# Kernel tuning notes

Hardware: AMD Instinct MI355X
Metric: run time of the kernel (lower is better)

## Reference

```python
import jax, jax.numpy as jnp
from jax import lax
import numpy as np

T, B, C, H, L, K = 512, 32, 512, 512, 2, 2  # time, batch, in_feat, hidden, layers, kernel


def setup_inputs() -> dict:
    key = jax.random.key(0)
    k0, k1, k2 = jax.random.split(key, 3)
    x = jax.random.normal(k0, (T, B, C), dtype=jnp.float32)
    # per layer: [n_dir=2, n_gate=4 (z,f,o,i), H, Cin, K] conv weights and [2,4,H] biases
    w0 = jax.random.normal(k1, (2, 4, H, C, K), dtype=jnp.float32) * 0.05
    b0 = jnp.zeros((2, 4, H), dtype=jnp.float32)
    w1 = jax.random.normal(k2, (2, 4, H, 2 * H, K), dtype=jnp.float32) * 0.05
    b1 = jnp.zeros((2, 4, H), dtype=jnp.float32)
    return {"x": x, "w0": w0, "b0": b0, "w1": w1, "b1": b1}


def _conv(x, w, b):
    # x: [B, Cin, T], w: [H, Cin, K]; left-pad K-1 zeros == torch cat([zeros, x]) + VALID conv
    y = lax.conv_general_dilated(x, w, (1,), [(K - 1, 0)],
                                 dimension_numbers=("NCH", "OIH", "NCH"))
    return y + b[None, :, None]


def _qrnn_layer(x, W, b, reverse):
    # x: [B, Cin, T]; W: [4, H, Cin, K]; b: [4, H]
    if reverse:
        x = x[:, :, ::-1]  # note: original code does NOT flip the output back
    z = jnp.tanh(_conv(x, W[0], b[0]))
    f = jax.nn.sigmoid(_conv(x, W[1], b[1]))  # eval-mode zoneout: 1-(1-sigmoid)=sigmoid
    o = jax.nn.sigmoid(_conv(x, W[2], b[2]))
    i = jax.nn.sigmoid(_conv(x, W[3], b[3]))
    iz = i * z
    f_t = jnp.moveaxis(f, 2, 0)   # [T, B, H]
    iz_t = jnp.moveaxis(iz, 2, 0)

    def step(c, fi):
        ft, izt = fi
        c = ft * c + izt  # IFO pooling recurrence
        return c, c

    _, cs = lax.scan(step, jnp.zeros(f_t.shape[1:], f.dtype), (f_t, iz_t))
    c = jnp.moveaxis(cs, 0, 2)  # [B, H, T]
    return o * c


def _forward(x, w0, b0, w1, b1):
    h = jnp.transpose(x, (1, 2, 0))  # [T,B,C] -> [B,C,T]
    h_lasts = []
    for W, bb in ((w0, b0), (w1, b1)):
        d0 = _qrnn_layer(h, W[0], bb[0], False)
        d1 = _qrnn_layer(h, W[1], bb[1], True)
        t_last = h.shape[2] - 2  # lengths.fill_(T-1); t_last = lengths - 1 = T-2 (faithful)
        h_lasts.append(jnp.concatenate([d0[:, :, t_last], d1[:, :, 0]], axis=1))  # [B, 2H]
        h = jnp.concatenate([d0, d1], axis=1)  # [B, 2H, T]
    output = jnp.transpose(h, (2, 0, 1))  # [T, B, 2H]
    h_n = jnp.stack(h_lasts, axis=0)      # [L, B, 2H]
    return output, h_n


def reference(x, w0, b0, w1, b1):
    return _forward(x, w0, b0, w1, b1)
```

## Files before the change

### kernel.cpp

```cpp
#include <hip/hip_runtime.h>
#include <cstddef>
#include <cstdint>

#define Tn 512
#define Bn 32
#define Hn 512
static const size_t PLANE = 8388608;

typedef float f32x4 __attribute__((ext_vector_type(4)));
typedef __bf16 bf16x8 __attribute__((ext_vector_type(8)));
typedef _Float16 h2 __attribute__((ext_vector_type(2)));

__device__ __forceinline__ float sigm(float x) { return 1.0f / (1.0f + __expf(-x)); }
__device__ __forceinline__ float tanh_fast(float x) { return 2.0f / (1.0f + __expf(-2.0f * x)) - 1.0f; }
__device__ __forceinline__ unsigned short f2bf(float f) {
    unsigned int u = __float_as_uint(f);
    u += 0x7FFF + ((u >> 16) & 1);
    return (unsigned short)(u >> 16);
}


__global__ __launch_bounds__(256) void conv_x(const float* __restrict__ x,
                                              unsigned short* __restrict__ xbf) {
    const int i = blockIdx.x * 256 + threadIdx.x;
    const int c8 = i & 63;
    const int tp = (i >> 6) % 514;
    const int b  = (i >> 6) / 514;
    unsigned short v[8];
    if (tp == 0 || tp == 513) {
#pragma unroll
        for (int j = 0; j < 8; ++j) v[j] = 0;
    } else {
        const float* s = x + ((size_t)(tp - 1) * Bn + b) * 512 + c8 * 8;
#pragma unroll
        for (int j = 0; j < 8; ++j) v[j] = f2bf(s[j]);
    }
    unsigned short* d = xbf + ((size_t)b * 514 + tp) * 512 + c8 * 8;
    *(uint4*)d = *(const uint4*)v;
}

__global__ __launch_bounds__(256) void conv_w(const float* __restrict__ src,
                                              unsigned short* __restrict__ dst,
                                              int Cin, int total) {
    const int i = blockIdx.x * 256 + threadIdx.x;
    if (i >= total) return;
    const int K = 2 * Cin;
    const int dm2 = i / K;
    const int kp = i - dm2 * K;
    const int dir = dm2 >> 11;
    const int mp = dm2 & 2047;
    const int o = mp >> 2;
    const int g = mp & 3;
    const int tap = (kp >= Cin) ? 1 : 0;
    const int c = kp - tap * Cin;
    dst[i] = f2bf(src[((((size_t)dir * 4 + g) * 512 + o) * Cin + c) * 2 + tap]);
}

__global__ __launch_bounds__(256) void zero_h1pad(unsigned short* __restrict__ h1bf) {
    const int i = blockIdx.x * 256 + threadIdx.x;
    const int c = i & 1023;
    const int b = (i >> 10) & 31;
    const int tp = (i >> 15) ? 513 : 0;
    h1bf[((size_t)b * 514 + tp) * 1024 + c] = 0;
}

template <int CIN>
__global__ __launch_bounds__(256) void gate_gemm_bf16(
    const unsigned short* __restrict__ Wbf,
    const unsigned short* __restrict__ Xbf,
    const float* __restrict__ bias,
    h2* __restrict__ fiz,
    _Float16* __restrict__ osb,
    int dir)
{
    __shared__ __align__(16) unsigned char smem[32768];
    unsigned short* As = (unsigned short*)smem;
    unsigned short* Bs = (unsigned short*)(smem + 16384);

    const int tid = threadIdx.x;
    const int lane = tid & 63;
    const int wave = tid >> 6;
    const int n0 = blockIdx.x * 128;
    const int m0 = blockIdx.y * 128;
    const int wm = (wave & 1) * 64;
    const int wn = (wave >> 1) * 64;

    const unsigned short* pA[4];
    const unsigned short* pB0[4];
    unsigned short* ldst[8];
#pragma unroll
    for (int r = 0; r < 4; ++r) {
        const int q = r * 256 + tid;
        const int row = q >> 3;
        const int j = q & 7;
        const int kk = j ^ ((row >> 1) & 7);
        pA[r] = Wbf + (size_t)(m0 + row) * (2 * CIN) + kk * 8;
        const int n = n0 + row;
        const int t = n & 511;
        const int b = n >> 9;
        const int tp0 = dir ? (513 - t) : t;
        pB0[r] = Xbf + ((size_t)b * 514 + tp0) * CIN + kk * 8;
        ldst[r] = As + (size_t)q * 8;
        ldst[r + 4] = Bs + (size_t)q * 8;
    }
    const int dstep = dir ? -CIN : CIN;

    int offA[2][4], offB[2][4];
#pragma unroll
    for (int kh = 0; kh < 2; ++kh) {
        const int jr = (lane >> 4) + kh * 4;
#pragma unroll
        for (int f = 0; f < 4; ++f) {
            const int ma = wm + f * 16 + (lane & 15);
            offA[kh][f] = ma * 64 + (jr ^ ((ma >> 1) & 7)) * 8;
            const int nb = wn + f * 16 + (lane & 15);
            offB[kh][f] = nb * 64 + (jr ^ ((nb >> 1) & 7)) * 8;
        }
    }

    f32x4 acc[4][4] = {};

    auto mfma_stage = [&]() {
#pragma unroll
        for (int kh = 0; kh < 2; ++kh) {
            bf16x8 af[4], bfr[4];
#pragma unroll
            for (int f = 0; f < 4; ++f) {
                af[f] = *(const bf16x8*)&As[offA[kh][f]];
                bfr[f] = *(const bf16x8*)&Bs[offB[kh][f]];
            }
#pragma unroll
            for (int fm = 0; fm < 4; ++fm)
#pragma unroll
                for (int fn = 0; fn < 4; ++fn)
                    acc[fm][fn] = __builtin_amdgcn_mfma_f32_16x16x32_bf16(
                        af[fm], bfr[fn], acc[fm][fn], 0, 0, 0);
        }
    };

#define GL(P, D) __builtin_amdgcn_global_load_lds( \
        (const __attribute__((address_space(1))) unsigned int*)(P), \
        (__attribute__((address_space(3))) unsigned int*)(D), 16, 0, 0)

#pragma unroll
    for (int tap = 0; tap < 2; ++tap) {
        const unsigned short* a0 = pA[0] + tap * CIN;
        const unsigned short* a1 = pA[1] + tap * CIN;
        const unsigned short* a2 = pA[2] + tap * CIN;
        const unsigned short* a3 = pA[3] + tap * CIN;
        const unsigned short* b0 = pB0[0] + tap * dstep;
        const unsigned short* b1 = pB0[1] + tap * dstep;
        const unsigned short* b2 = pB0[2] + tap * dstep;
        const unsigned short* b3 = pB0[3] + tap * dstep;
#pragma unroll
        for (int s = 0; s < CIN / 64; ++s) {
            GL(a0, ldst[0]); GL(a1, ldst[1]);
            GL(a2, ldst[2]); GL(a3, ldst[3]);
            GL(b0, ldst[4]); GL(b1, ldst[5]);
            GL(b2, ldst[6]); GL(b3, ldst[7]);
            __builtin_amdgcn_s_waitcnt(0);
            __syncthreads();
            mfma_stage();
            __syncthreads();
            a0 += 64; a1 += 64; a2 += 64; a3 += 64;
            b0 += 64; b1 += 64; b2 += 64; b3 += 64;
        }
    }
#undef GL

    const int q = lane >> 4;
    const int o0 = blockIdx.y * 32;
    float Bz[4], Bf[4], Bo[4], Bi[4];
#pragma unroll
    for (int fm = 0; fm < 4; ++fm) {
        const int o = o0 + (wm >> 2) + fm * 4 + q;
        Bz[fm] = bias[o];
        Bf[fm] = bias[512 + o];
        Bo[fm] = bias[1024 + o];
        Bi[fm] = bias[1536 + o];
    }
    h2* Lfiz = (h2*)smem;
    _Float16* Los = (_Float16*)(smem + 18432);
#pragma unroll
    for (int fm = 0; fm < 4; ++fm) {
        const int ol = (wm >> 2) + fm * 4 + q;
#pragma unroll
        for (int fn = 0; fn < 4; ++fn) {
            f32x4 v = acc[fm][fn];
            const float f  = sigm(v.y + Bf[fm]);
            const float iz = sigm(v.w + Bi[fm]) * tanh_fast(v.x + Bz[fm]);
            const float os = sigm(v.z + Bo[fm]);
            const int nl = wn + fn * 16 + (lane & 15);
            h2 p; p.x = (_Float16)f; p.y = (_Float16)iz;
            Lfiz[nl * 36 + ol] = p;
            Los[nl * 40 + ol] = (_Float16)os;
        }
    }
    __syncthreads();
#pragma unroll
    for (int l = 0; l < 4; ++l) {
        const int idx = l * 256 + tid;
        const int row = idx >> 3;
        const int col = idx & 7;
        uint4 v = *(const uint4*)((const unsigned char*)smem + row * 144 + col * 16);
        ((uint4*)(fiz + (size_t)(n0 + row) * 512 + o0))[col] = v;
    }
#pragma unroll
    for (int l = 0; l < 2; ++l) {
        const int idx = l * 256 + tid;
        const int row = idx >> 2;
        const int col = idx & 3;
        uint4 v = *(const uint4*)((const unsigned char*)smem + 18432 + row * 80 + col * 16);
        ((uint4*)(osb + (size_t)(n0 + row) * 512 + o0))[col] = v;
    }
}


__global__ __launch_bounds__(256) void scan_A(
    const h2* __restrict__ fiz,
    float* __restrict__ Fsum, float* __restrict__ Ssum)
{
    const int idx = blockIdx.x * 256 + threadIdx.x;
    const int o = idx & 511;
    const int b = (idx >> 9) & 31;
    const int chunk = idx >> 14;
    float F = 1.0f, S = 0.0f;
    const int tbase = chunk * 64;
    for (int tt = 0; tt < 64; ++tt) {
        const h2 v = fiz[((size_t)(b * 512 + tbase + tt)) * 512 + o];
        const float f = (float)v.x;
        const float iz = (float)v.y;
        F *= f;
        S = f * S + iz;
    }
    Fsum[idx] = F;
    Ssum[idx] = S;
}

__global__ __launch_bounds__(256) void scan_B(
    const float* __restrict__ Fsum, const float* __restrict__ Ssum,
    float* __restrict__ cstart)
{
    const int i = blockIdx.x * 256 + threadIdx.x;
    float c = 0.0f;
    for (int ch = 0; ch < 8; ++ch) {
        cstart[ch * 16384 + i] = c;
        c = Fsum[ch * 16384 + i] * c + Ssum[ch * 16384 + i];
    }
}

__global__ __launch_bounds__(256) void scan_C(
    const h2* __restrict__ fiz, const _Float16* __restrict__ osb,
    const float* __restrict__ cstart, float* __restrict__ out,
    unsigned short* __restrict__ h1bf,
    float* __restrict__ hn, int isLayer2, int dirH)
{
    const int idx = blockIdx.x * 256 + threadIdx.x;
    const int o = idx & 511;
    const int b = (idx >> 9) & 31;
    const int chunk = idx >> 14;
    float c = cstart[idx];
    const int tbase = chunk * 64;
    for (int tt = 0; tt < 64; ++tt) {
        const int t = tbase + tt;
        const size_t idxg = ((size_t)(b * 512 + t)) * 512 + o;
        const h2 v = fiz[idxg];
        const float f = (float)v.x;
        const float iz = (float)v.y;
        const float os = (float)osb[idxg];
        c = f * c + iz;
        const float outv = os * c;
        if (isLayer2) {
            out[((size_t)t * Bn + b) * 1024 + dirH + o] = outv;
        } else {
            h1bf[((size_t)b * 514 + (t + 1)) * 1024 + dirH + o] = f2bf(outv);
        }
        const bool isLast = (dirH == 0) ? (t == Tn - 2) : (t == 0);
        if (isLast) hn[(size_t)b * 1024 + dirH + o] = outv;
    }
}

extern "C" void kernel_launch(void* const* d_in, const int* in_sizes, int n_in,
                              void* d_out, int out_size, void* d_ws, size_t ws_size,
                              hipStream_t stream) {
    const float* x  = (const float*)d_in[0];
    const float* w0 = (const float*)d_in[1];
    const float* b0 = (const float*)d_in[2];
    const float* w1 = (const float*)d_in[3];
    const float* b1 = (const float*)d_in[4];
    float* out = (float*)d_out;
    float* ws = (float*)d_ws;

    h2* fiz        = (h2*)ws;
    _Float16* osb  = (_Float16*)(ws + PLANE);
    float* Fsum    = ws + PLANE + PLANE / 2;
    float* Ssum    = Fsum + 131072;
    float* cst     = Ssum + 131072;
    unsigned short* xbf  = (unsigned short*)(cst + 131072);
    unsigned short* h1bf = xbf + (size_t)32 * 514 * 512;
    unsigned short* w0bf = h1bf + (size_t)32 * 514 * 1024;
    unsigned short* w1bf = w0bf + (size_t)2 * 2048 * 1024;
    float* hn = out + 16777216;

    conv_x<<<4112, 256, 0, stream>>>(x, xbf);
    conv_w<<<16384, 256, 0, stream>>>(w0, w0bf, 512, 4194304);
    conv_w<<<32768, 256, 0, stream>>>(w1, w1bf, 1024, 8388608);
    zero_h1pad<<<256, 256, 0, stream>>>(h1bf);

    const dim3 gg(128, 16);

    gate_gemm_bf16<512><<<gg, 256, 0, stream>>>(w0bf, xbf, b0, fiz, osb, 0);
    scan_A<<<512, 256, 0, stream>>>(fiz, Fsum, Ssum);
    scan_B<<<64, 256, 0, stream>>>(Fsum, Ssum, cst);
    scan_C<<<512, 256, 0, stream>>>(fiz, osb, cst, out, h1bf, hn, 0, 0);
    gate_gemm_bf16<512><<<gg, 256, 0, stream>>>(w0bf + (size_t)2048 * 1024, xbf, b0 + 2048, fiz, osb, 1);
    scan_A<<<512, 256, 0, stream>>>(fiz, Fsum, Ssum);
    scan_B<<<64, 256, 0, stream>>>(Fsum, Ssum, cst);
    scan_C<<<512, 256, 0, stream>>>(fiz, osb, cst, out, h1bf, hn, 0, 512);
    gate_gemm_bf16<1024><<<gg, 256, 0, stream>>>(w1bf, h1bf, b1, fiz, osb, 0);
    scan_A<<<512, 256, 0, stream>>>(fiz, Fsum, Ssum);
    scan_B<<<64, 256, 0, stream>>>(Fsum, Ssum, cst);
    scan_C<<<512, 256, 0, stream>>>(fiz, osb, cst, out, h1bf, hn + 32768, 1, 0);
    gate_gemm_bf16<1024><<<gg, 256, 0, stream>>>(w1bf + (size_t)2048 * 2048, h1bf, b1 + 2048, fiz, osb, 1);
    scan_A<<<512, 256, 0, stream>>>(fiz, Fsum, Ssum);
    scan_B<<<64, 256, 0, stream>>>(Fsum, Ssum, cst);
    scan_C<<<512, 256, 0, stream>>>(fiz, osb, cst, out, h1bf, hn + 32768, 1, 512);
}
```

Baseline: 696.4 us.

## Batch both directions per layer and fuse chunk-scan reduction into gate GEMM

```diff
diff --git a/kernel.cpp b/kernel.cpp
--- a/kernel.cpp
+++ b/kernel.cpp
@@ -39,11 +39,16 @@
     *(uint4*)d = *(const uint4*)v;
 }
 
-__global__ __launch_bounds__(256) void conv_w(const float* __restrict__ src,
-                                              unsigned short* __restrict__ dst,
-                                              int Cin, int total) {
-    const int i = blockIdx.x * 256 + threadIdx.x;
-    if (i >= total) return;
+__global__ __launch_bounds__(256) void conv_w2(const float* __restrict__ w0,
+                                               const float* __restrict__ w1,
+                                               unsigned short* __restrict__ w0bf,
+                                               unsigned short* __restrict__ w1bf) {
+    int i = blockIdx.x * 256 + threadIdx.x;
+    const float* src;
+    unsigned short* dst;
+    int Cin;
+    if (i < 4194304) { src = w0; dst = w0bf; Cin = 512; }
+    else { i -= 4194304; src = w1; dst = w1bf; Cin = 1024; }
     const int K = 2 * Cin;
     const int dm2 = i / K;
     const int kp = i - dm2 * K;
@@ -71,7 +76,8 @@
     const float* __restrict__ bias,
     h2* __restrict__ fiz,
     _Float16* __restrict__ osb,
-    int dir)
+    float* __restrict__ Fsum,
+    float* __restrict__ Ssum)
 {
     __shared__ __align__(16) unsigned char smem[32768];
     unsigned short* As = (unsigned short*)smem;
@@ -81,9 +87,12 @@
     const int lane = tid & 63;
     const int wave = tid >> 6;
     const int n0 = blockIdx.x * 128;
-    const int m0 = blockIdx.y * 128;
+    const int dir = blockIdx.y >> 4;
+    const int m0 = (blockIdx.y & 15) * 128;
     const int wm = (wave & 1) * 64;
     const int wn = (wave >> 1) * 64;
+
+    const unsigned short* Wb = Wbf + (size_t)dir * 2048 * 2 * CIN;
 
     const unsigned short* pA[4];
     const unsigned short* pB0[4];
@@ -94,7 +103,7 @@
         const int row = q >> 3;
         const int j = q & 7;
         const int kk = j ^ ((row >> 1) & 7);
-        pA[r] = Wbf + (size_t)(m0 + row) * (2 * CIN) + kk * 8;
+        pA[r] = Wb + (size_t)(m0 + row) * (2 * CIN) + kk * 8;
         const int n = n0 + row;
         const int t = n & 511;
         const int b = n >> 9;
@@ -169,15 +178,16 @@
 #undef GL
 
     const int q = lane >> 4;
-    const int o0 = blockIdx.y * 32;
+    const int o0 = (blockIdx.y & 15) * 32;
+    const float* bb = bias + dir * 2048;
     float Bz[4], Bf[4], Bo[4], Bi[4];
 #pragma unroll
     for (int fm = 0; fm < 4; ++fm) {
         const int o = o0 + (wm >> 2) + fm * 4 + q;
-        Bz[fm] = bias[o];
-        Bf[fm] = bias[512 + o];
-        Bo[fm] = bias[1024 + o];
-        Bi[fm] = bias[1536 + o];
+        Bz[fm] = bb[o];
+        Bf[fm] = bb[512 + o];
+        Bo[fm] = bb[1024 + o];
+        Bi[fm] = bb[1536 + o];
     }
     h2* Lfiz = (h2*)smem;
     _Float16* Los = (_Float16*)(smem + 18432);
@@ -197,13 +207,15 @@
         }
     }
     __syncthreads();
+    h2* fz = fiz + (size_t)dir * PLANE;
+    _Float16* ob = osb + (size_t)dir * PLANE;
 #pragma unroll
     for (int l = 0; l < 4; ++l) {
         const int idx = l * 256 + tid;
         const int row = idx >> 3;
         const int col = idx & 7;
         uint4 v = *(const uint4*)((const unsigned char*)smem + row * 144 + col * 16);
-        ((uint4*)(fiz + (size_t)(n0 + row) * 512 + o0))[col] = v;
+        ((uint4*)(fz + (size_t)(n0 + row) * 512 + o0))[col] = v;
     }
 #pragma unroll
     for (int l = 0; l < 2; ++l) {
@@ -211,41 +223,39 @@
         const int row = idx >> 2;
         const int col = idx & 3;
         uint4 v = *(const uint4*)((const unsigned char*)smem + 18432 + row * 80 + col * 16);
-        ((uint4*)(osb + (size_t)(n0 + row) * 512 + o0))[col] = v;
-    }
-}
-
-
-__global__ __launch_bounds__(256) void scan_A(
-    const h2* __restrict__ fiz,
-    float* __restrict__ Fsum, float* __restrict__ Ssum)
-{
-    const int idx = blockIdx.x * 256 + threadIdx.x;
-    const int o = idx & 511;
-    const int b = (idx >> 9) & 31;
-    const int chunk = idx >> 14;
-    float F = 1.0f, S = 0.0f;
-    const int tbase = chunk * 64;
-    for (int tt = 0; tt < 64; ++tt) {
-        const h2 v = fiz[((size_t)(b * 512 + tbase + tt)) * 512 + o];
-        const float f = (float)v.x;
-        const float iz = (float)v.y;
-        F *= f;
-        S = f * S + iz;
-    }
-    Fsum[idx] = F;
-    Ssum[idx] = S;
-}
+        ((uint4*)(ob + (size_t)(n0 + row) * 512 + o0))[col] = v;
+    }
+    if (tid < 64) {
+        const int ol = tid & 31;
+        const int ch = tid >> 5;
+        float F = 1.0f, S = 0.0f;
+#pragma unroll
+        for (int tt = 0; tt < 64; ++tt) {
+            const h2 v = Lfiz[(ch * 64 + tt) * 36 + ol];
+            const float f = (float)v.x;
+            F *= f;
+            S = f * S + (float)v.y;
+        }
+        const int b = n0 >> 9;
+        const int chg = ((n0 & 511) >> 6) + ch;
+        const int o = o0 + ol;
+        const int sidx = dir * 131072 + chg * 16384 + b * 512 + o;
+        Fsum[sidx] = F;
+        Ssum[sidx] = S;
+    }
+}
+
 
 __global__ __launch_bounds__(256) void scan_B(
     const float* __restrict__ Fsum, const float* __restrict__ Ssum,
     float* __restrict__ cstart)
 {
     const int i = blockIdx.x * 256 + threadIdx.x;
+    const int base = (i >> 14) * 131072 + (i & 16383);
     float c = 0.0f;
     for (int ch = 0; ch < 8; ++ch) {
-        cstart[ch * 16384 + i] = c;
-        c = Fsum[ch * 16384 + i] * c + Ssum[ch * 16384 + i];
+        cstart[base + ch * 16384] = c;
+        c = Fsum[base + ch * 16384] * c + Ssum[base + ch * 16384];
     }
 }
 
@@ -253,21 +263,26 @@
     const h2* __restrict__ fiz, const _Float16* __restrict__ osb,
     const float* __restrict__ cstart, float* __restrict__ out,
     unsigned short* __restrict__ h1bf,
-    float* __restrict__ hn, int isLayer2, int dirH)
+    float* __restrict__ hn, int isLayer2)
 {
     const int idx = blockIdx.x * 256 + threadIdx.x;
-    const int o = idx & 511;
-    const int b = (idx >> 9) & 31;
-    const int chunk = idx >> 14;
+    const int dir = idx >> 17;
+    const int rem = idx & 131071;
+    const int o = rem & 511;
+    const int b = (rem >> 9) & 31;
+    const int chunk = rem >> 14;
+    const int dirH = dir * 512;
     float c = cstart[idx];
+    const h2* fz = fiz + (size_t)dir * PLANE;
+    const _Float16* ob = osb + (size_t)dir * PLANE;
     const int tbase = chunk * 64;
     for (int tt = 0; tt < 64; ++tt) {
         const int t = tbase + tt;
         const size_t idxg = ((size_t)(b * 512 + t)) * 512 + o;
-        const h2 v = fiz[idxg];
+        const h2 v = fz[idxg];
         const float f = (float)v.x;
         const float iz = (float)v.y;
-        const float os = (float)osb[idxg];
+        const float os = (float)ob[idxg];
         c = f * c + iz;
         const float outv = os * c;
         if (isLayer2) {
@@ -275,7 +290,7 @@
         } else {
             h1bf[((size_t)b * 514 + (t + 1)) * 1024 + dirH + o] = f2bf(outv);
         }
-        const bool isLast = (dirH == 0) ? (t == Tn - 2) : (t == 0);
+        const bool isLast = (dir == 0) ? (t == Tn - 2) : (t == 0);
         if (isLast) hn[(size_t)b * 1024 + dirH + o] = outv;
     }
 }
@@ -292,37 +307,26 @@
     float* ws = (float*)d_ws;
 
     h2* fiz        = (h2*)ws;
-    _Float16* osb  = (_Float16*)(ws + PLANE);
-    float* Fsum    = ws + PLANE + PLANE / 2;
-    float* Ssum    = Fsum + 131072;
-    float* cst     = Ssum + 131072;
-    unsigned short* xbf  = (unsigned short*)(cst + 131072);
+    _Float16* osb  = (_Float16*)(ws + 16777216);
+    float* Fsum    = ws + 16777216 + 8388608;
+    float* Ssum    = Fsum + 262144;
+    float* cst     = Ssum + 262144;
+    unsigned short* xbf  = (unsigned short*)(cst + 262144);
     unsigned short* h1bf = xbf + (size_t)32 * 514 * 512;
     unsigned short* w0bf = h1bf + (size_t)32 * 514 * 1024;
     unsigned short* w1bf = w0bf + (size_t)2 * 2048 * 1024;
     float* hn = out + 16777216;
 
     conv_x<<<4112, 256, 0, stream>>>(x, xbf);
-    conv_w<<<16384, 256, 0, stream>>>(w0, w0bf, 512, 4194304);
-    conv_w<<<32768, 256, 0, stream>>>(w1, w1bf, 1024, 8388608);
+    conv_w2<<<49152, 256, 0, stream>>>(w0, w1, w0bf, w1bf);
     zero_h1pad<<<256, 256, 0, stream>>>(h1bf);
 
-    const dim3 gg(128, 16);
-
-    gate_gemm_bf16<512><<<gg, 256, 0, stream>>>(w0bf, xbf, b0, fiz, osb, 0);
-    scan_A<<<512, 256, 0, stream>>>(fiz, Fsum, Ssum);
-    scan_B<<<64, 256, 0, stream>>>(Fsum, Ssum, cst);
-    scan_C<<<512, 256, 0, stream>>>(fiz, osb, cst, out, h1bf, hn, 0, 0);
-    gate_gemm_bf16<512><<<gg, 256, 0, stream>>>(w0bf + (size_t)2048 * 1024, xbf, b0 + 2048, fiz, osb, 1);
-    scan_A<<<512, 256, 0, stream>>>(fiz, Fsum, Ssum);
-    scan_B<<<64, 256, 0, stream>>>(Fsum, Ssum, cst);
-    scan_C<<<512, 256, 0, stream>>>(fiz, osb, cst, out, h1bf, hn, 0, 512);
-    gate_gemm_bf16<1024><<<gg, 256, 0, stream>>>(w1bf, h1bf, b1, fiz, osb, 0);
-    scan_A<<<512, 256, 0, stream>>>(fiz, Fsum, Ssum);
-    scan_B<<<64, 256, 0, stream>>>(Fsum, Ssum, cst);
-    scan_C<<<512, 256, 0, stream>>>(fiz, osb, cst, out, h1bf, hn + 32768, 1, 0);
-    gate_gemm_bf16<1024><<<gg, 256, 0, stream>>>(w1bf + (size_t)2048 * 2048, h1bf, b1 + 2048, fiz, osb, 1);
-    scan_A<<<512, 256, 0, stream>>>(fiz, Fsum, Ssum);
-    scan_B<<<64, 256, 0, stream>>>(Fsum, Ssum, cst);
-    scan_C<<<512, 256, 0, stream>>>(fiz, osb, cst, out, h1bf, hn + 32768, 1, 512);
-}
+    const dim3 gg(128, 32);
+
+    gate_gemm_bf16<512><<<gg, 256, 0, stream>>>(w0bf, xbf, b0, fiz, osb, Fsum, Ssum);
+    scan_B<<<128, 256, 0, stream>>>(Fsum, Ssum, cst);
+    scan_C<<<1024, 256, 0, stream>>>(fiz, osb, cst, out, h1bf, hn, 0);
+    gate_gemm_bf16<1024><<<gg, 256, 0, stream>>>(w1bf, h1bf, b1, fiz, osb, Fsum, Ssum);
+    scan_B<<<128, 256, 0, stream>>>(Fsum, Ssum, cst);
+    scan_C<<<1024, 256, 0, stream>>>(fiz, osb, cst, out, h1bf, hn + 32768, 1);
+}
```

After: 635.2 us. 1.1x faster.
